# Kernel optimization log

Measured on AMD Instinct MI355X. Metric: run time of the kernel, lower is better.

Reference implementation:

```python
import jax, jax.numpy as jnp
import numpy as np

HIDDEN = 2048
NUM_Q_HEADS = 32
NUM_KV_HEADS = 8
HEAD_DIM = HIDDEN // NUM_Q_HEADS  # 64
GROUPS = NUM_Q_HEADS // NUM_KV_HEADS  # 4
MAX_WAVELENGTH = 10000.0
B, S = 2, 1024
NEG_INF = -1e9  # keras Softmax masking constant


def apply_rope(x, start_index=0, max_wavelength=MAX_WAVELENGTH):
    # x: [b, s, h, d]; keras_hub RotaryEmbedding (split-half / Llama style)
    d = x.shape[-1]
    s = x.shape[1]
    freq_range = jnp.arange(0, d, 2, dtype=jnp.float32)
    inverse_freq = 1.0 / (max_wavelength ** (freq_range / d))  # [d/2]
    positions = jnp.arange(s, dtype=jnp.float32) + start_index
    freq = positions[:, None] * inverse_freq[None, :]  # [s, d/2]
    emb = jnp.concatenate([freq, freq], axis=-1)[None, :, None, :]  # [1,s,1,d]
    cos = jnp.cos(emb).astype(x.dtype)
    sin = jnp.sin(emb).astype(x.dtype)
    x1, x2 = jnp.split(x, 2, axis=-1)
    half_rot = jnp.concatenate([-x2, x1], axis=-1)
    return x * cos + half_rot * sin


def setup_inputs() -> dict:
    key = jax.random.key(0)
    k1, k2, k3, k4, k5 = jax.random.split(key, 5)
    hidden_states = jax.random.normal(k1, (B, S, HIDDEN), dtype=jnp.float32)
    # causal mask, broadcast over batch
    attention_mask = jnp.broadcast_to(
        jnp.tril(jnp.ones((S, S), dtype=bool))[None], (B, S, S)
    )
    scale = 1.0 / np.sqrt(HIDDEN)
    Wq = jax.random.normal(k2, (HIDDEN, NUM_Q_HEADS * HEAD_DIM), dtype=jnp.float32) * scale
    Wk = jax.random.normal(k3, (HIDDEN, NUM_KV_HEADS * HEAD_DIM), dtype=jnp.float32) * scale
    Wv = jax.random.normal(k4, (HIDDEN, NUM_KV_HEADS * HEAD_DIM), dtype=jnp.float32) * scale
    Wo = jax.random.normal(k5, (NUM_Q_HEADS * HEAD_DIM, HIDDEN), dtype=jnp.float32) * scale
    return {"hidden_states": hidden_states, "attention_mask": attention_mask,
            "Wq": Wq, "Wk": Wk, "Wv": Wv, "Wo": Wo}


def reference(hidden_states, attention_mask, Wq, Wk, Wv, Wo):
    b, s, _ = hidden_states.shape
    q = (hidden_states @ Wq).reshape(b, s, NUM_Q_HEADS, HEAD_DIM)
    k = (hidden_states @ Wk).reshape(b, s, NUM_KV_HEADS, HEAD_DIM)
    v = (hidden_states @ Wv).reshape(b, s, NUM_KV_HEADS, HEAD_DIM)
    q = apply_rope(q)
    k = apply_rope(k)
    # GQA: repeat kv heads to match query heads (ops.repeat on axis 2)
    k = jnp.repeat(k, GROUPS, axis=2)
    v = jnp.repeat(v, GROUPS, axis=2)
    inv_norm = 1.0 / np.sqrt(HEAD_DIM)
    scores = jnp.einsum("bquh,bkuh->buqk", q, k) * inv_norm  # [b, h, q, k]
    scores = scores.astype(jnp.float32)
    scores = jnp.where(attention_mask[:, None, :, :], scores, NEG_INF)
    probs = jax.nn.softmax(scores, axis=-1).astype(hidden_states.dtype)
    attn = jnp.einsum("buqk,bkuh->bquh", probs, v)  # [b, q, h, hd]
    attn = attn.reshape(b, s, HIDDEN)
    return attn @ Wo
```

## Files before the change

kernel.cpp:

```cpp
#include <hip/hip_runtime.h>
#include <hip/hip_bf16.h>
#include <math.h>

#define S_LEN 1024
#define BATCH 2
#define HIDDEN 2048
#define NQH 32
#define NKVH 8
#define HD 64
#define LDQKV 3072
#define M_ROWS (BATCH * S_LEN)

typedef __attribute__((ext_vector_type(8))) short bf16x8;
typedef __attribute__((ext_vector_type(4))) float f32x4;

typedef unsigned int uint32_g __attribute__((address_space(1)));
typedef unsigned int uint32_l __attribute__((address_space(3)));

static __device__ __forceinline__ void load_lds16(const void* g, void* l) {
    __builtin_amdgcn_global_load_lds((const uint32_g*)g, (uint32_l*)l, 16, 0, 0);
}

static __device__ __forceinline__ short f2bf(float f) {
    union { __hip_bfloat16 h; short s; } cv;
    cv.h = __float2bfloat16(f);
    return cv.s;
}

__global__ __launch_bounds__(256) void conv_all_kernel(
    const float* __restrict__ X,
    const float* __restrict__ Wq, const float* __restrict__ Wk,
    const float* __restrict__ Wv, const float* __restrict__ Wo,
    short* __restrict__ Xb, short* __restrict__ Wqkvt, short* __restrict__ Wot,
    float2* __restrict__ cs2)
{
    __shared__ short Ts[64][68];
    const int tid = threadIdx.x;

    if (blockIdx.z == 4) {
        int flat = blockIdx.y * 32 + blockIdx.x;
        size_t base = (size_t)flat * 4096 + (size_t)tid * 16;
        #pragma unroll
        for (int rep = 0; rep < 2; ++rep) {
            size_t i = base + rep * 8;
            float4 a = *reinterpret_cast<const float4*>(X + i);
            float4 b = *reinterpret_cast<const float4*>(X + i + 4);
            union { bf16x8 v; short s[8]; } t;
            t.s[0] = f2bf(a.x); t.s[1] = f2bf(a.y); t.s[2] = f2bf(a.z); t.s[3] = f2bf(a.w);
            t.s[4] = f2bf(b.x); t.s[5] = f2bf(b.y); t.s[6] = f2bf(b.z); t.s[7] = f2bf(b.w);
            *reinterpret_cast<bf16x8*>(Xb + i) = t.v;
        }
        if (flat < 128) {
            int g = flat * 256 + tid;
            int s = g >> 5, i = g & 31;
            float inv_freq = 1.0f / powf(10000.0f, (float)i / 32.0f);
            float freq = (float)s * inv_freq;
            double sn, cs;
            sincos((double)freq, &sn, &cs);
            cs2[g] = make_float2((float)cs, (float)sn);
        }
        return;
    }

    const float* src; short* dst; int N;
    switch (blockIdx.z) {
        case 0: src = Wq; dst = Wqkvt;                         N = 2048; break;
        case 1: src = Wk; dst = Wqkvt + (size_t)2048 * 2048;   N = 512;  break;
        case 2: src = Wv; dst = Wqkvt + (size_t)2560 * 2048;   N = 512;  break;
        default: src = Wo; dst = Wot;                          N = 2048; break;
    }
    const int n0 = blockIdx.x * 64, k0 = blockIdx.y * 64;
    if (n0 >= N) return;

    #pragma unroll
    for (int rep = 0; rep < 4; ++rep) {
        int idx = rep * 256 + tid;
        int row = idx >> 4, c4 = (idx & 15) * 4;
        float4 v = *reinterpret_cast<const float4*>(
            src + (size_t)(k0 + row) * N + n0 + c4);
        ushort4 u;
        u.x = (unsigned short)f2bf(v.x); u.y = (unsigned short)f2bf(v.y);
        u.z = (unsigned short)f2bf(v.z); u.w = (unsigned short)f2bf(v.w);
        *reinterpret_cast<ushort4*>(&Ts[row][c4]) = u;
    }
    __syncthreads();
    #pragma unroll
    for (int rep = 0; rep < 2; ++rep) {
        int idx = rep * 256 + tid;
        int n = idx >> 3, kc = (idx & 7) * 8;
        union { bf16x8 v; short s[8]; } t;
        #pragma unroll
        for (int j = 0; j < 8; ++j) t.s[j] = Ts[kc + j][n];
        *reinterpret_cast<bf16x8*>(dst + (size_t)(n0 + n) * 2048 + k0 + kc) = t.v;
    }
}

template <bool ROPE_BF16>
__global__ __launch_bounds__(256) void gemm_bf16_kernel(
    const short* __restrict__ A, const short* __restrict__ Bt,
    float* __restrict__ C, short* __restrict__ Cb,
    short* __restrict__ vt_g,
    const float2* __restrict__ cs2, int K, int ldc)
{
    const int n0 = blockIdx.x * 64, m0 = blockIdx.y * 128;
    const int tid = threadIdx.x;
    const int w = tid >> 6, lane = tid & 63;
    const int m15 = lane & 15, q4 = lane >> 4;

    __shared__ short SL[2][128 * 64 + 64 * 64];

    f32x4 acc[2][4];
    #pragma unroll
    for (int i = 0; i < 2; ++i)
        #pragma unroll
        for (int j = 0; j < 4; ++j) acc[i][j] = (f32x4){0.f, 0.f, 0.f, 0.f};

    const int srow = lane >> 3;
    const int pchunk = lane & 7;

#define GSTAGE(bf_, k0_) do {                                                 \
    short (*As_)[64] = (short(*)[64])SL[bf_];                                 \
    short (*Bs_)[64] = (short(*)[64])(SL[bf_] + 128 * 64);                    \
    _Pragma("unroll")                                                         \
    for (int r = 0; r < 4; ++r) {                                             \
        int row = (w * 4 + r) * 8 + srow;                         \
        int lchunk = pchunk ^ (row & 7);                                      \
        load_lds16(A + (size_t)(m0 + row) * K + (k0_) + lchunk * 8,           \
                   &As_[(w * 4 + r) * 8][0]);                                 \
    }                                                                         \
    _Pragma("unroll")                                                         \
    for (int r = 0; r < 2; ++r) {                                             \
        int row = (w * 2 + r) * 8 + srow;                          \
        int lchunk = pchunk ^ (row & 7);                                      \
        load_lds16(Bt + (size_t)(n0 + row) * K + (k0_) + lchunk * 8,          \
                   &Bs_[(w * 2 + r) * 8][0]);                                 \
    }                                                                         \
} while (0)

    GSTAGE(0, 0);
    __syncthreads();

    const int nkt = K >> 6;
    for (int kt = 0; kt < nkt; ++kt) {
        const int bf = kt & 1;
        if (kt + 1 < nkt) GSTAGE(bf ^ 1, (kt + 1) * 64);

        short (*As)[64] = (short(*)[64])SL[bf];
        short (*Bs)[64] = (short(*)[64])(SL[bf] + 128 * 64);
        #pragma unroll
        for (int ch = 0; ch < 2; ++ch) {
            bf16x8 af[2], bff[4];
            #pragma unroll
            for (int mt = 0; mt < 2; ++mt) {
                int row = w * 32 + mt * 16 + m15;
                af[mt] = *reinterpret_cast<const bf16x8*>(
                    &As[row][(((ch * 4 + q4) ^ (row & 7))) * 8]);
            }
            #pragma unroll
            for (int nt = 0; nt < 4; ++nt) {
                int row = nt * 16 + m15;
                bff[nt] = *reinterpret_cast<const bf16x8*>(
                    &Bs[row][(((ch * 4 + q4) ^ (row & 7))) * 8]);
            }
            #pragma unroll
            for (int mt = 0; mt < 2; ++mt)
                #pragma unroll
                for (int nt = 0; nt < 4; ++nt)
                    acc[mt][nt] = __builtin_amdgcn_mfma_f32_16x16x32_bf16(
                        af[mt], bff[nt], acc[mt][nt], 0, 0, 0);
        }
        __syncthreads();
    }
#undef GSTAGE

    if (!ROPE_BF16) {
        #pragma unroll
        for (int mt = 0; mt < 2; ++mt)
            #pragma unroll
            for (int nt = 0; nt < 4; ++nt)
                #pragma unroll
                for (int reg = 0; reg < 4; ++reg)
                    C[(size_t)(m0 + w * 32 + mt * 16 + q4 * 4 + reg) * ldc
                      + n0 + nt * 16 + m15] = acc[mt][nt][reg];
    } else if (n0 < 2560) {
        #pragma unroll
        for (int mt = 0; mt < 2; ++mt) {
            #pragma unroll
            for (int reg = 0; reg < 4; ++reg) {
                int row = m0 + w * 32 + mt * 16 + q4 * 4 + reg;
                int s = row & (S_LEN - 1);
                float2 t0 = cs2[s * 32 + m15];
                float2 t1 = cs2[s * 32 + 16 + m15];
                float a0 = acc[mt][0][reg], a1 = acc[mt][1][reg];
                float a2 = acc[mt][2][reg], a3 = acc[mt][3][reg];
                size_t base = (size_t)row * ldc + n0 + m15;
                Cb[base +  0] = f2bf(a0 * t0.x - a2 * t0.y);
                Cb[base + 16] = f2bf(a1 * t1.x - a3 * t1.y);
                Cb[base + 32] = f2bf(a2 * t0.x + a0 * t0.y);
                Cb[base + 48] = f2bf(a3 * t1.x + a1 * t1.y);
            }
        }
    } else {
        __syncthreads();
        short (*VT)[136] = (short(*)[136])SL[0];
        #pragma unroll
        for (int mt = 0; mt < 2; ++mt) {
            #pragma unroll
            for (int nt = 0; nt < 4; ++nt) {
                ushort4 u;
                u.x = (unsigned short)f2bf(acc[mt][nt][0]);
                u.y = (unsigned short)f2bf(acc[mt][nt][1]);
                u.z = (unsigned short)f2bf(acc[mt][nt][2]);
                u.w = (unsigned short)f2bf(acc[mt][nt][3]);
                *reinterpret_cast<ushort4*>(
                    &VT[nt * 16 + m15][w * 32 + mt * 16 + q4 * 4]) = u;
            }
        }
        __syncthreads();
        const int kvh = (n0 - 2560) >> 6;
        const int b = m0 >> 10, k0loc = m0 & (S_LEN - 1);
        const int dim = tid >> 2, kc = (tid & 3) * 32;
        short* dst = vt_g + (size_t)((b * 8 + kvh) * 64 + dim) * S_LEN + k0loc + kc;
        #pragma unroll
        for (int u = 0; u < 4; ++u)
            *reinterpret_cast<bf16x8*>(dst + u * 8) =
                *reinterpret_cast<const bf16x8*>(&VT[dim][kc + u * 8]);
    }
}

__global__ __launch_bounds__(512) void attn_kernel(
    const short* __restrict__ qkvb, const short* __restrict__ vt_g,
    short* __restrict__ attn_b)
{
    const int i  = blockIdx.x;
    const int h  = blockIdx.y;
    const int b  = blockIdx.z;
    const int qtA = i;
    const int qtB = 15 - i;
    const int tid = threadIdx.x;
    const int w = tid >> 6, lane = tid & 63;
    const int kvh = h >> 2;
    const int m15 = lane & 15, q4 = lane >> 4;

    __shared__ short Ks[2][64][64];
    __shared__ short Vt[2][64][64];
    __shared__ float Ps[8][16][68];

    const int qt_w = (w < 4) ? qtB : qtA;
    const int rowbase = qt_w * 64 + (w & 3) * 16;

    const bf16x8 qf0 = *reinterpret_cast<const bf16x8*>(
        qkvb + (size_t)(b * S_LEN + rowbase + m15) * LDQKV + h * HD + q4 * 8);
    const bf16x8 qf1 = *reinterpret_cast<const bf16x8*>(
        qkvb + (size_t)(b * S_LEN + rowbase + m15) * LDQKV + h * HD + 32 + q4 * 8);

    f32x4 o4[4];
    #pragma unroll
    for (int k = 0; k < 4; ++k) o4[k] = (f32x4){0.f, 0.f, 0.f, 0.f};
    float lsum[4] = {0.f, 0.f, 0.f, 0.f};

    const int r8 = lane >> 3, p8 = lane & 7;
    const int lch = (p8 ^ r8) * 8;
    const short* kbase = qkvb + (size_t)(b * S_LEN) * LDQKV + 2048 + kvh * HD;
    const short* vbase = vt_g + (size_t)(b * 8 + kvh) * 64 * S_LEN;

#define STAGE(bf_, t) do {                                                    \
    int row_ = w * 8 + r8;                                                    \
    load_lds16(kbase + (size_t)((t) * 64 + row_) * LDQKV + lch,               \
               &Ks[bf_][w * 8][0]);                                           \
    load_lds16(vbase + (size_t)row_ * S_LEN + (t) * 64 + lch,                 \
               &Vt[bf_][w * 8][0]);                                           \
} while (0)

#define COMPUTE(bf_, t) do {                                                  \
    const int xr_ = m15 & 7;                                                  \
    bf16x8 pf_[2];                                                            \
    _Pragma("unroll")                                                         \
    for (int nt = 0; nt < 4; ++nt) {                                          \
        f32x4 acc = (f32x4){0.f, 0.f, 0.f, 0.f};                              \
        bf16x8 kf0 = *reinterpret_cast<const bf16x8*>(                        \
            &Ks[bf_][nt * 16 + m15][(q4 ^ xr_) * 8]);                         \
        bf16x8 kf1 = *reinterpret_cast<const bf16x8*>(                        \
            &Ks[bf_][nt * 16 + m15][((4 + q4) ^ xr_) * 8]);                   \
        acc = __builtin_amdgcn_mfma_f32_16x16x32_bf16(qf0, kf0, acc, 0, 0, 0);\
        acc = __builtin_amdgcn_mfma_f32_16x16x32_bf16(qf1, kf1, acc, 0, 0, 0);\
        int colg = (t) * 64 + nt * 16 + m15;                                  \
        _Pragma("unroll")                                                     \
        for (int reg = 0; reg < 4; ++reg) {                                   \
            int rowg = rowbase + q4 * 4 + reg;                                \
            float p = (colg <= rowg)                                          \
                ? exp2f(fminf(acc[reg] * 0.180336880f, 80.f)) : 0.f;          \
            lsum[reg] += p;                                                   \
            Ps[w][q4 * 4 + reg][nt * 16 + m15] = p;                           \
        }                                                                     \
    }                                                                         \
    _Pragma("unroll")                                                         \
    for (int ch = 0; ch < 2; ++ch) {                                          \
        f32x4 pa = *reinterpret_cast<const f32x4*>(                           \
            &Ps[w][m15][ch * 32 + q4 * 8]);                                   \
        f32x4 pb = *reinterpret_cast<const f32x4*>(                           \
            &Ps[w][m15][ch * 32 + q4 * 8 + 4]);                               \
        union { bf16x8 v; short s[8]; } tb;                                   \
        tb.s[0] = f2bf(pa[0]); tb.s[1] = f2bf(pa[1]);                         \
        tb.s[2] = f2bf(pa[2]); tb.s[3] = f2bf(pa[3]);                         \
        tb.s[4] = f2bf(pb[0]); tb.s[5] = f2bf(pb[1]);                         \
        tb.s[6] = f2bf(pb[2]); tb.s[7] = f2bf(pb[3]);                         \
        pf_[ch] = tb.v;                                                       \
    }                                                                         \
    _Pragma("unroll")                                                         \
    for (int nt2 = 0; nt2 < 4; ++nt2) {                                       \
        bf16x8 vf0 = *reinterpret_cast<const bf16x8*>(                        \
            &Vt[bf_][nt2 * 16 + m15][(q4 ^ xr_) * 8]);                        \
        bf16x8 vf1 = *reinterpret_cast<const bf16x8*>(                        \
            &Vt[bf_][nt2 * 16 + m15][((4 + q4) ^ xr_) * 8]);                  \
        o4[nt2] = __builtin_amdgcn_mfma_f32_16x16x32_bf16(                    \
            pf_[0], vf0, o4[nt2], 0, 0, 0);                                   \
        o4[nt2] = __builtin_amdgcn_mfma_f32_16x16x32_bf16(                    \
            pf_[1], vf1, o4[nt2], 0, 0, 0);                                   \
    }                                                                         \
} while (0)

    STAGE(0, 0);
    __syncthreads();

    for (int t = 0; t <= qtB; ++t) {
        const int bf = t & 1;
        if (t < qtB) STAGE(bf ^ 1, t + 1);
        if (t <= qt_w) COMPUTE(bf, t);
        __syncthreads();
    }

#undef STAGE
#undef COMPUTE

    float invl[4];
    #pragma unroll
    for (int reg = 0; reg < 4; ++reg) {
        float l = lsum[reg];
        l += __shfl_xor(l, 1, 64);
        l += __shfl_xor(l, 2, 64);
        l += __shfl_xor(l, 4, 64);
        l += __shfl_xor(l, 8, 64);
        invl[reg] = 1.0f / l;
    }

    #pragma unroll
    for (int nt2 = 0; nt2 < 4; ++nt2)
        #pragma unroll
        for (int reg = 0; reg < 4; ++reg)
            attn_b[(size_t)(b * S_LEN + rowbase + q4 * 4 + reg) * HIDDEN
                   + h * HD + nt2 * 16 + m15] = f2bf(o4[nt2][reg] * invl[reg]);
}

extern "C" void kernel_launch(void* const* d_in, const int* in_sizes, int n_in,
                              void* d_out, int out_size, void* d_ws, size_t ws_size,
                              hipStream_t stream) {
    const float* X  = (const float*)d_in[0];
    const float* Wq = (const float*)d_in[2];
    const float* Wk = (const float*)d_in[3];
    const float* Wv = (const float*)d_in[4];
    const float* Wo = (const float*)d_in[5];
    float* out = (float*)d_out;

    short*  qkvb  = (short*)d_ws;
    short*  Xb    = qkvb + (size_t)M_ROWS * LDQKV;
    short*  Wqkvt = Xb + (size_t)HIDDEN * HIDDEN;
    short*  Wot   = Wqkvt + (size_t)LDQKV * HIDDEN;
    short*  vt_g  = Wot + (size_t)HIDDEN * HIDDEN;
    float2* cs2   = (float2*)(vt_g + (size_t)16 * 64 * S_LEN);
    short*  attn_b = Xb;

    conv_all_kernel<<<dim3(32, 32, 5), dim3(256), 0, stream>>>(
        X, Wq, Wk, Wv, Wo, Xb, Wqkvt, Wot, cs2);

    gemm_bf16_kernel<true><<<dim3(48, 16), dim3(256), 0, stream>>>(
        Xb, Wqkvt, nullptr, qkvb, vt_g, cs2, 2048, LDQKV);
    attn_kernel<<<dim3(8, 32, 2), dim3(512), 0, stream>>>(qkvb, vt_g, attn_b);
    gemm_bf16_kernel<false><<<dim3(32, 16), dim3(256), 0, stream>>>(
        attn_b, Wot, out, nullptr, nullptr, nullptr, 2048, HIDDEN);
}
```

Measured before the change: 194.5 us.

## Transpose QK^T MFMA and pass probabilities via shuffles instead of LDS

Swaps the MFMA operands so scores come out transposed (keys along registers, queries along lanes). Each lane then packs its own bf16 probabilities and builds the P operand for the PV MFMA with cross-lane shuffles, replacing the LDS scratch buffer and its write/read round trip. The causal mask is only evaluated on diagonal tiles, the row sum becomes a single scalar reduced across lane groups, and launch bounds now request higher occupancy. This trades LDS traffic and shared memory for 16 shuffles per tile, with possible register pressure from the occupancy hint.

```diff
diff --git a/kernel.cpp b/kernel.cpp
--- a/kernel.cpp
+++ b/kernel.cpp
@@ -228,7 +228,7 @@
     }
 }
 
-__global__ __launch_bounds__(512) void attn_kernel(
+__global__ __launch_bounds__(512, 4) void attn_kernel(
     const short* __restrict__ qkvb, const short* __restrict__ vt_g,
     short* __restrict__ attn_b)
 {
@@ -244,7 +244,6 @@
 
     __shared__ short Ks[2][64][64];
     __shared__ short Vt[2][64][64];
-    __shared__ float Ps[8][16][68];
 
     const int qt_w = (w < 4) ? qtB : qtA;
     const int rowbase = qt_w * 64 + (w & 3) * 16;
@@ -257,7 +256,7 @@
     f32x4 o4[4];
     #pragma unroll
     for (int k = 0; k < 4; ++k) o4[k] = (f32x4){0.f, 0.f, 0.f, 0.f};
-    float lsum[4] = {0.f, 0.f, 0.f, 0.f};
+    float lsum = 0.f;
 
     const int r8 = lane >> 3, p8 = lane & 7;
     const int lch = (p8 ^ r8) * 8;
@@ -274,7 +273,7 @@
 
 #define COMPUTE(bf_, t) do {                                                  \
     const int xr_ = m15 & 7;                                                  \
-    bf16x8 pf_[2];                                                            \
+    float p_[4][4];                                                           \
     _Pragma("unroll")                                                         \
     for (int nt = 0; nt < 4; ++nt) {                                          \
         f32x4 acc = (f32x4){0.f, 0.f, 0.f, 0.f};                              \
@@ -282,30 +281,53 @@
             &Ks[bf_][nt * 16 + m15][(q4 ^ xr_) * 8]);                         \
         bf16x8 kf1 = *reinterpret_cast<const bf16x8*>(                        \
             &Ks[bf_][nt * 16 + m15][((4 + q4) ^ xr_) * 8]);                   \
-        acc = __builtin_amdgcn_mfma_f32_16x16x32_bf16(qf0, kf0, acc, 0, 0, 0);\
-        acc = __builtin_amdgcn_mfma_f32_16x16x32_bf16(qf1, kf1, acc, 0, 0, 0);\
-        int colg = (t) * 64 + nt * 16 + m15;                                  \
+        acc = __builtin_amdgcn_mfma_f32_16x16x32_bf16(kf0, qf0, acc, 0, 0, 0);\
+        acc = __builtin_amdgcn_mfma_f32_16x16x32_bf16(kf1, qf1, acc, 0, 0, 0);\
         _Pragma("unroll")                                                     \
-        for (int reg = 0; reg < 4; ++reg) {                                   \
-            int rowg = rowbase + q4 * 4 + reg;                                \
-            float p = (colg <= rowg)                                          \
-                ? exp2f(fminf(acc[reg] * 0.180336880f, 80.f)) : 0.f;          \
-            lsum[reg] += p;                                                   \
-            Ps[w][q4 * 4 + reg][nt * 16 + m15] = p;                           \
-        }                                                                     \
-    }                                                                         \
+        for (int reg = 0; reg < 4; ++reg)                                     \
+            p_[nt][reg] = exp2f(fminf(acc[reg] * 0.180336880f, 80.f));        \
+    }                                                                         \
+    if ((t) * 64 + 63 > rowbase) {            \
+        const int rowg_ = rowbase + m15;                                      \
+        _Pragma("unroll")                                                     \
+        for (int nt = 0; nt < 4; ++nt)                                        \
+            _Pragma("unroll")                                                 \
+            for (int reg = 0; reg < 4; ++reg)                                 \
+                if ((t) * 64 + nt * 16 + q4 * 4 + reg > rowg_)                \
+                    p_[nt][reg] = 0.f;                                        \
+    }                                                                         \
+    _Pragma("unroll")                                                         \
+    for (int nt = 0; nt < 4; ++nt)                                            \
+        _Pragma("unroll")                                                     \
+        for (int reg = 0; reg < 4; ++reg) lsum += p_[nt][reg];                \
+    unsigned lo_[4], hi_[4];                                                  \
+    _Pragma("unroll")                                                         \
+    for (int nt = 0; nt < 4; ++nt) {                                          \
+        lo_[nt] = (unsigned)(unsigned short)f2bf(p_[nt][0])                   \
+                | ((unsigned)(unsigned short)f2bf(p_[nt][1]) << 16);          \
+        hi_[nt] = (unsigned)(unsigned short)f2bf(p_[nt][2])                   \
+                | ((unsigned)(unsigned short)f2bf(p_[nt][3]) << 16);          \
+    }                                                                         \
+    const int La_ = ((q4 & 1) * 2) * 16 + m15;                                \
+    const int Lb_ = La_ + 16;                                                 \
+    const int hiH_ = q4 >> 1;                                                 \
+    bf16x8 pf_[2];                                                            \
     _Pragma("unroll")                                                         \
     for (int ch = 0; ch < 2; ++ch) {                                          \
-        f32x4 pa = *reinterpret_cast<const f32x4*>(                           \
-            &Ps[w][m15][ch * 32 + q4 * 8]);                                   \
-        f32x4 pb = *reinterpret_cast<const f32x4*>(                           \
-            &Ps[w][m15][ch * 32 + q4 * 8 + 4]);                               \
-        union { bf16x8 v; short s[8]; } tb;                                   \
-        tb.s[0] = f2bf(pa[0]); tb.s[1] = f2bf(pa[1]);                         \
-        tb.s[2] = f2bf(pa[2]); tb.s[3] = f2bf(pa[3]);                         \
-        tb.s[4] = f2bf(pb[0]); tb.s[5] = f2bf(pb[1]);                         \
-        tb.s[6] = f2bf(pb[2]); tb.s[7] = f2bf(pb[3]);                         \
-        pf_[ch] = tb.v;                                                       \
+        int a0 = __shfl((int)lo_[ch * 2],     La_, 64);                       \
+        int a1 = __shfl((int)hi_[ch * 2],     La_, 64);                       \
+        int a2 = __shfl((int)lo_[ch * 2],     Lb_, 64);                       \
+        int a3 = __shfl((int)hi_[ch * 2],     Lb_, 64);                       \
+        int b0 = __shfl((int)lo_[ch * 2 + 1], La_, 64);                       \
+        int b1 = __shfl((int)hi_[ch * 2 + 1], La_, 64);                       \
+        int b2 = __shfl((int)lo_[ch * 2 + 1], Lb_, 64);                       \
+        int b3 = __shfl((int)hi_[ch * 2 + 1], Lb_, 64);                       \
+        union { int ii[4]; bf16x8 v; } u_;                                    \
+        u_.ii[0] = hiH_ ? b0 : a0;                                            \
+        u_.ii[1] = hiH_ ? b1 : a1;                                            \
+        u_.ii[2] = hiH_ ? b2 : a2;                                            \
+        u_.ii[3] = hiH_ ? b3 : a3;                                            \
+        pf_[ch] = u_.v;                                                       \
     }                                                                         \
     _Pragma("unroll")                                                         \
     for (int nt2 = 0; nt2 < 4; ++nt2) {                                       \
@@ -333,23 +355,21 @@
 #undef STAGE
 #undef COMPUTE
 
-    float invl[4];
-    #pragma unroll
-    for (int reg = 0; reg < 4; ++reg) {
-        float l = lsum[reg];
-        l += __shfl_xor(l, 1, 64);
-        l += __shfl_xor(l, 2, 64);
-        l += __shfl_xor(l, 4, 64);
-        l += __shfl_xor(l, 8, 64);
-        invl[reg] = 1.0f / l;
-    }
+    float l = lsum;
+    l += __shfl_xor(l, 16, 64);
+    l += __shfl_xor(l, 32, 64);
+    float invl = 1.0f / l;
+    float invl4[4];
+    #pragma unroll
+    for (int reg = 0; reg < 4; ++reg)
+        invl4[reg] = __shfl(invl, q4 * 4 + reg, 64);
 
     #pragma unroll
     for (int nt2 = 0; nt2 < 4; ++nt2)
         #pragma unroll
         for (int reg = 0; reg < 4; ++reg)
             attn_b[(size_t)(b * S_LEN + rowbase + q4 * 4 + reg) * HIDDEN
-                   + h * HD + nt2 * 16 + m15] = f2bf(o4[nt2][reg] * invl[reg]);
+                   + h * HD + nt2 * 16 + m15] = f2bf(o4[nt2][reg] * invl4[reg]);
 }
 
 extern "C" void kernel_launch(void* const* d_in, const int* in_sizes, int n_in,
```

Measured after the change: 194.7 us (median of 2 runs). No clear change (+0.1%).
